# Kernel tuning notes

Hardware: AMD Instinct MI355X
Metric: run time of the kernel (lower is better)

The kernel has to match this reference:

```python
import jax, jax.numpy as jnp
import numpy as np

# SparseSphereConv (graph_level=6 -> V=40962, kernel_size=9, stride=1, select_index=None)
# Pipeline: neighbor gather -> data-dependent nonzero row selection ->
# per-vertex KxK interpolation matmul -> 1xK conv (linear over C_in,K) -> scatter back.
# With stride=1 / select_index=None the static selection is the identity, so the
# dynamic nonzero selection is equivalent to computing all rows and zeroing the
# rows whose gathered features are entirely zero (selected rows are scattered back,
# unselected rows stay 0 in sparse_reset's zero-initialized output).

BS, C_IN, C_OUT, V, K = 4, 32, 32, 40962, 9

def setup_inputs() -> dict:
    key = jax.random.key(0)
    k1, k2, k3, k4, k5 = jax.random.split(key, 5)
    x = jax.random.normal(k1, (BS, C_IN, V), dtype=jnp.float32)
    index = jax.random.randint(k2, (V, K), 0, V, dtype=jnp.int32)          # neighbor ids per vertex
    itp_mat = jax.random.uniform(k3, (V, K, K), dtype=jnp.float32)         # per-vertex interpolation
    conv_w = jax.random.normal(k4, (C_OUT, C_IN, K), dtype=jnp.float32) * 0.05  # Conv2d(C_in,C_out,(1,K)) weight
    conv_b = jax.random.normal(k5, (C_OUT,), dtype=jnp.float32) * 0.05
    return {"x": x, "index": index, "itp_mat": itp_mat, "conv_w": conv_w, "conv_b": conv_b}

def reference(x, index, itp_mat, conv_w, conv_b):
    # x: [bs, C, V] -> permute(2,0,1) -> gather neighbors -> [V, K, bs, C]
    g = jnp.transpose(x, (2, 0, 1))[index]
    g = jnp.transpose(g, (3, 2, 0, 1))                      # [C, bs, V, K]  (== reshape of [C, bs*V, K])
    # sparse_prepare: keep rows whose min or max over (C, K) is nonzero (detached in torch)
    gd = jax.lax.stop_gradient(g)
    rmin = gd.min(axis=(0, 3))                              # [bs, V]
    rmax = gd.max(axis=(0, 3))                              # [bs, V]
    mask = (rmin != 0) | (rmax != 0)                        # [bs, V]
    # Interploate: [C, S, 1, K] @ [S, K, K] per row -> batched small matmul
    interp = jnp.einsum('cbvk,vkj->cbvj', g, itp_mat)       # [C, bs, V, K]
    # Conv2d with kernel (1, K): contraction over (C_in, K) + bias
    out = jnp.einsum('cbvk,ock->bov', interp, conv_w) + conv_b[None, :, None]  # [bs, C_out, V]
    # sparse_reset: rows not selected stay zero
    return out * mask[:, None, :].astype(out.dtype)
```

## Files before the change

### kernel.cpp

```cpp
#include <hip/hip_runtime.h>

#define NV 40962
#define NK 9
#define CIN 32
#define COUT 32
#define NBS 4
#define VT 256
#define TP 260
#define NT 2561
#define PGRID 512
#define NV81 (NV * 81)
#define NV9  (NV * 9)

typedef __attribute__((ext_vector_type(8))) short bf16x8;
typedef __attribute__((ext_vector_type(4))) float f32x4;

__device__ __forceinline__ unsigned bf16pair(float a, float b) {
    unsigned ua = __float_as_uint(a), ub = __float_as_uint(b);
    ua = (ua + 0x7FFFu + ((ua >> 16) & 1u)) >> 16;
    ub = (ub + 0x7FFFu + ((ub >> 16) & 1u)) & 0xFFFF0000u;
    return (ua & 0xFFFFu) | ub;
}

__device__ __forceinline__ void bar_lgkm() {
    asm volatile("s_waitcnt lgkmcnt(0)\n\ts_barrier" ::: "memory");
}

__global__ void __launch_bounds__(256) transpose_x_bf16(
    const float* __restrict__ x, unsigned* __restrict__ xtw)
{
    __shared__ unsigned T[16 * TP];
    const int b  = blockIdx.x & 3;
    const int v0 = (blockIdx.x >> 2) * VT;
    const int t  = threadIdx.x;
    const int w  = t >> 6;
    const int L  = t & 63;
    const bool full = (v0 + VT <= NV);

    #pragma unroll
    for (int i = 0; i < 4; ++i) {
        const int q = w + 4 * i;
        const float* rowA = x + (size_t)(b * 32 + 2 * q) * NV;
        const float* rowB = rowA + NV;
        #pragma unroll
        for (int h = 0; h < 2; ++h) {
            const int vl = 128 * h + 2 * L;
            float2 a, c;
            if (full) {
                a = *(const float2*)(rowA + v0 + vl);
                c = *(const float2*)(rowB + v0 + vl);
            } else {
                const int v = v0 + vl;
                a.x = (v     < NV) ? rowA[v]     : 0.0f;
                a.y = (v + 1 < NV) ? rowA[v + 1] : 0.0f;
                c.x = (v     < NV) ? rowB[v]     : 0.0f;
                c.y = (v + 1 < NV) ? rowB[v + 1] : 0.0f;
            }
            uint2 d;
            d.x = bf16pair(a.x, c.x);
            d.y = bf16pair(a.y, c.y);
            *(uint2*)&T[q * TP + vl] = d;
        }
    }
    __syncthreads();

    #pragma unroll
    for (int i = 0; i < 4; ++i) {
        const int vl = i * 64 + w * 16 + (L >> 2);
        const int u4 = L & 3;
        const int v  = v0 + vl;
        if (v < NV) {
            uint4 d;
            d.x = T[(4 * u4 + 0) * TP + vl];
            d.y = T[(4 * u4 + 1) * TP + vl];
            d.z = T[(4 * u4 + 2) * TP + vl];
            d.w = T[(4 * u4 + 3) * TP + vl];
            *(uint4*)&xtw[(size_t)v * 64 + b * 16 + 4 * u4] = d;
        }
    }
}

__device__ __forceinline__ void load_itp(float itpv[3],
                                         const float* __restrict__ itp,
                                         int tile, int t)
{
    const size_t base = (size_t)tile * 1296;
    #pragma unroll
    for (int i = 0; i < 3; ++i) {
        const int o = i * 512 + t;
        itpv[i] = (o < 1296 && base + o < (size_t)NV81) ? itp[base + o] : 0.0f;
    }
}

__device__ __forceinline__ void stage_itp(float* __restrict__ buf,
                                          const float itpv[3], int t)
{
    #pragma unroll
    for (int i = 0; i < 3; ++i) {
        const int o = i * 512 + t;
        if (o < 1296) {
            const int vl = o / 81;
            const int r  = o - vl * 81;
            const int kk = r / 9;
            const int jj = r - kk * 9;
            buf[vl * 108 + kk * 12 + jj] = itpv[i];
        }
    }
}

__device__ __forceinline__ int load_idx(const int* __restrict__ index,
                                        int tile, int t)
{
    int r = 0;
    if (t < 144) {
        const size_t base = (size_t)tile * 144 + t;
        r = (base < (size_t)NV9) ? index[base] : 0;
    }
    return r;
}

__global__ void __launch_bounds__(512) sparse_conv_mfma(
    const unsigned short* __restrict__ xt, const int* __restrict__ index,
    const float* __restrict__ itp, const float* __restrict__ w,
    const float* __restrict__ bias, float* __restrict__ out)
{
    __shared__ unsigned short Alds[36 * 64 * 8];
    __shared__ unsigned short Wlds[36 * 32 * 8];
    __shared__ float itp_s[16 * 108];
    __shared__ int   idx_s[2][144];
    __shared__ unsigned nzv[8][64];

    const int t    = threadIdx.x;
    const int col  = t & 63;
    const int q    = t >> 6;
    const int b    = col >> 4;
    const int vloc = col & 15;
    const unsigned short* gb = xt + b * 32 + q * 4;

    int tile = blockIdx.x;

    #pragma unroll
    for (int r = 0; r < 3; ++r) {
        const int j = t + r * 512;
        if (j < 1152) {
            const int o = j & 31;
            const int c = j >> 5;
            const float4 f0 = *(const float4*)(w + o * 288 + c * 8);
            const float4 f1 = *(const float4*)(w + o * 288 + c * 8 + 4);
            uint4 d;
            d.x = bf16pair(f0.x, f0.y); d.y = bf16pair(f0.z, f0.w);
            d.z = bf16pair(f1.x, f1.y); d.w = bf16pair(f1.z, f1.w);
            *(uint4*)&Wlds[(c * 32 + o) * 8] = d;
        }
    }
    {
        const int i0 = load_idx(index, tile, t);
        const int i1 = load_idx(index, min(tile + PGRID, NT - 1), t);
        if (t < 144) { idx_s[0][t] = i0; idx_s[1][t] = i1; }
    }
    float itpv[3];
    load_itp(itpv, itp, tile, t);
    stage_itp(itp_s, itpv, t);
    bar_lgkm();

    uint2 gath[NK];
    #pragma unroll
    for (int k = 0; k < NK; ++k) {
        const int nbr = idx_s[0][vloc * 9 + k];
        gath[k] = *(const uint2*)(gb + (size_t)nbr * 128);
    }
    load_itp(itpv, itp, min(tile + PGRID, NT - 1), t);
    int idxn = load_idx(index, min(tile + 2 * PGRID, NT - 1), t);
    int cur = 0;

    for (; tile < NT; tile += PGRID) {
        unsigned nzbits = 0;
        float acc[4][NK];
        #pragma unroll
        for (int cc = 0; cc < 4; ++cc)
            #pragma unroll
            for (int j = 0; j < NK; ++j) acc[cc][j] = 0.0f;
        #pragma unroll
        for (int k = 0; k < NK; ++k) {
            const unsigned lo = gath[k].x, hi = gath[k].y;
            nzbits |= (lo | hi) & 0x7FFF7FFFu;
            const float g0 = __uint_as_float(lo << 16);
            const float g1 = __uint_as_float(lo & 0xFFFF0000u);
            const float g2 = __uint_as_float(hi << 16);
            const float g3 = __uint_as_float(hi & 0xFFFF0000u);
            const float4 ra = *(const float4*)&itp_s[vloc * 108 + k * 12];
            const float4 rb = *(const float4*)&itp_s[vloc * 108 + k * 12 + 4];
            const float  r8 = itp_s[vloc * 108 + k * 12 + 8];
            const float row[NK] = {ra.x, ra.y, ra.z, ra.w,
                                   rb.x, rb.y, rb.z, rb.w, r8};
            #pragma unroll
            for (int j = 0; j < NK; ++j) {
                acc[0][j] += g0 * row[j];
                acc[1][j] += g1 * row[j];
                acc[2][j] += g2 * row[j];
                acc[3][j] += g3 * row[j];
            }
        }
        #pragma unroll
        for (int i2 = 0; i2 < 9; ++i2) {
            const int k0 = 4 * i2;
            const int chunk = (9 * q + i2) >> 1;
            const int off = 4 * ((q + i2) & 1);
            uint2 d;
            d.x = bf16pair(acc[k0 / 9][k0 % 9],
                           acc[(k0 + 1) / 9][(k0 + 1) % 9]);
            d.y = bf16pair(acc[(k0 + 2) / 9][(k0 + 2) % 9],
                           acc[(k0 + 3) / 9][(k0 + 3) % 9]);
            *(uint2*)&Alds[(chunk * 64 + col) * 8 + off] = d;
        }
        nzv[q][col] = nzbits;

        #pragma unroll
        for (int k = 0; k < NK; ++k) {
            const int nbr = idx_s[cur ^ 1][vloc * 9 + k];
            gath[k] = *(const uint2*)(gb + (size_t)nbr * 128);
        }

        bar_lgkm();

        {
            const int dn = vloc;
            const int dq = col >> 4;
            const int bb = q >> 1;
            const int oh = q & 1;
            const int colw = bb * 16 + dn;

            f32x4 a0 = {0.f, 0.f, 0.f, 0.f};
            #pragma unroll
            for (int ks = 0; ks < 9; ++ks) {
                const int ch = ks * 4 + dq;
                const bf16x8 wa = *(const bf16x8*)&Wlds[(ch * 32 + oh * 16 + dn) * 8];
                const bf16x8 bf = *(const bf16x8*)&Alds[(ch * 64 + colw) * 8];
                a0 = __builtin_amdgcn_mfma_f32_16x16x32_bf16(wa, bf, a0, 0, 0, 0);
            }

            const unsigned nz = nzv[0][colw] | nzv[1][colw] |
                                nzv[2][colw] | nzv[3][colw] |
                                nzv[4][colw] | nzv[5][colw] |
                                nzv[6][colw] | nzv[7][colw];
            const float m = nz ? 1.0f : 0.0f;
            const int vv = tile * 16 + dn;
            if (vv < NV) {
                float* outb = out + (size_t)bb * (COUT * NV) + vv;
                #pragma unroll
                for (int r = 0; r < 4; ++r) {
                    const int o = oh * 16 + dq * 4 + r;
                    outb[(size_t)o * NV] = (a0[r] + bias[o]) * m;
                }
            }
        }
        stage_itp(itp_s, itpv, t);
        if (t < 144) idx_s[cur][t] = idxn;
        load_itp(itpv, itp, min(tile + 2 * PGRID, NT - 1), t);
        idxn = load_idx(index, min(tile + 3 * PGRID, NT - 1), t);

        bar_lgkm();
        cur ^= 1;
    }
}

extern "C" void kernel_launch(void* const* d_in, const int* in_sizes, int n_in,
                              void* d_out, int out_size, void* d_ws, size_t ws_size,
                              hipStream_t stream)
{
    const float* x     = (const float*)d_in[0];
    const int*   index = (const int*)  d_in[1];
    const float* itp   = (const float*)d_in[2];
    const float* w     = (const float*)d_in[3];
    const float* bias  = (const float*)d_in[4];
    float*       out   = (float*)d_out;

    unsigned short* xt = (unsigned short*)d_ws;

    const int vtiles = (NV + VT - 1) / VT;
    hipLaunchKernelGGL(transpose_x_bf16, dim3(vtiles * NBS), dim3(256), 0,
                       stream, x, (unsigned*)xt);
    hipLaunchKernelGGL(sparse_conv_mfma, dim3(PGRID), dim3(512), 0,
                       stream, xt, index, itp, w, bias, out);
}
```

Measured before the change: 139.7 us.

## Stage neighbor gathers via direct global-to-LDS DMA and keep weights in registers

Replaces the per-thread register gathers of neighbor rows with global_load_lds DMA into a double-buffered padded LDS tile, prefetching the next tile's rows while the current one is computed. Conv weight fragments move from LDS into per-thread registers, index storage shrinks to 16-bit, and the nonzero mask is reduced with a wave ballot instead of a per-lane LDS array. The persistent grid drops from 512 to 256 blocks to fit the larger LDS footprint. The trade-off is lower occupancy and a full barrier per iteration, plus higher register use from the weight fragments.

```diff
diff --git a/kernel.cpp b/kernel.cpp
--- a/kernel.cpp
+++ b/kernel.cpp
@@ -8,7 +8,8 @@
 #define VT 256
 #define TP 260
 #define NT 2561
-#define PGRID 512
+#define PGRID 256
+#define GROW 66
 #define NV81 (NV * 81)
 #define NV9  (NV * 9)
 
@@ -24,6 +25,12 @@
 
 __device__ __forceinline__ void bar_lgkm() {
     asm volatile("s_waitcnt lgkmcnt(0)\n\ts_barrier" ::: "memory");
+}
+
+__device__ __forceinline__ void dma_row4(const unsigned* g, unsigned* l) {
+    __builtin_amdgcn_global_load_lds(
+        (const __attribute__((address_space(1))) unsigned*)g,
+        (__attribute__((address_space(3))) unsigned*)l, 4, 0, 0);
 }
 
 __global__ void __launch_bounds__(256) transpose_x_bf16(
@@ -124,56 +131,65 @@
     const float* __restrict__ itp, const float* __restrict__ w,
     const float* __restrict__ bias, float* __restrict__ out)
 {
+    __shared__ unsigned Glds[2][144 * GROW];
     __shared__ unsigned short Alds[36 * 64 * 8];
-    __shared__ unsigned short Wlds[36 * 32 * 8];
     __shared__ float itp_s[16 * 108];
-    __shared__ int   idx_s[2][144];
-    __shared__ unsigned nzv[8][64];
+    __shared__ unsigned short idx_s[2][144];
+    __shared__ unsigned long long nzb[8];
 
     const int t    = threadIdx.x;
     const int col  = t & 63;
     const int q    = t >> 6;
     const int b    = col >> 4;
     const int vloc = col & 15;
-    const unsigned short* gb = xt + b * 32 + q * 4;
+    const unsigned* xtw = (const unsigned*)xt;
+
+    bf16x8 wfr[9];
+    {
+        const int o = (q & 1) * 16 + vloc;
+        const float* wo = w + o * 288 + b * 8;
+        #pragma unroll
+        for (int ks = 0; ks < 9; ++ks) {
+            const float4 f0 = *(const float4*)(wo + ks * 32);
+            const float4 f1 = *(const float4*)(wo + ks * 32 + 4);
+            union { uint4 u; bf16x8 v; } cv;
+            cv.u.x = bf16pair(f0.x, f0.y); cv.u.y = bf16pair(f0.z, f0.w);
+            cv.u.z = bf16pair(f1.x, f1.y); cv.u.w = bf16pair(f1.z, f1.w);
+            wfr[ks] = cv.v;
+        }
+    }
 
     int tile = blockIdx.x;
-
-    #pragma unroll
-    for (int r = 0; r < 3; ++r) {
-        const int j = t + r * 512;
-        if (j < 1152) {
-            const int o = j & 31;
-            const int c = j >> 5;
-            const float4 f0 = *(const float4*)(w + o * 288 + c * 8);
-            const float4 f1 = *(const float4*)(w + o * 288 + c * 8 + 4);
-            uint4 d;
-            d.x = bf16pair(f0.x, f0.y); d.y = bf16pair(f0.z, f0.w);
-            d.z = bf16pair(f1.x, f1.y); d.w = bf16pair(f1.z, f1.w);
-            *(uint4*)&Wlds[(c * 32 + o) * 8] = d;
-        }
-    }
     {
         const int i0 = load_idx(index, tile, t);
         const int i1 = load_idx(index, min(tile + PGRID, NT - 1), t);
-        if (t < 144) { idx_s[0][t] = i0; idx_s[1][t] = i1; }
+        if (t < 144) { idx_s[0][t] = (unsigned short)i0;
+                       idx_s[1][t] = (unsigned short)i1; }
     }
     float itpv[3];
     load_itp(itpv, itp, tile, t);
     stage_itp(itp_s, itpv, t);
-    bar_lgkm();
-
-    uint2 gath[NK];
-    #pragma unroll
-    for (int k = 0; k < NK; ++k) {
-        const int nbr = idx_s[0][vloc * 9 + k];
-        gath[k] = *(const uint2*)(gb + (size_t)nbr * 128);
+    __syncthreads();
+
+    #pragma unroll
+    for (int r = 0; r < 18; ++r) {
+        const int row = q * 18 + r;
+        const int nbr = idx_s[0][row];
+        dma_row4(xtw + (size_t)nbr * 64 + col, &Glds[0][row * GROW]);
     }
     load_itp(itpv, itp, min(tile + PGRID, NT - 1), t);
     int idxn = load_idx(index, min(tile + 2 * PGRID, NT - 1), t);
-    int cur = 0;
-
+    __syncthreads();
+
+    int g = 0, cur = 0;
     for (; tile < NT; tile += PGRID) {
+        #pragma unroll
+        for (int r = 0; r < 18; ++r) {
+            const int row = q * 18 + r;
+            const int nbr = idx_s[cur ^ 1][row];
+            dma_row4(xtw + (size_t)nbr * 64 + col, &Glds[g ^ 1][row * GROW]);
+        }
+
         unsigned nzbits = 0;
         float acc[4][NK];
         #pragma unroll
@@ -182,7 +198,8 @@
             for (int j = 0; j < NK; ++j) acc[cc][j] = 0.0f;
         #pragma unroll
         for (int k = 0; k < NK; ++k) {
-            const unsigned lo = gath[k].x, hi = gath[k].y;
+            const unsigned* p = &Glds[g][(vloc * 9 + k) * GROW + b * 16 + q * 2];
+            const unsigned lo = p[0], hi = p[1];
             nzbits |= (lo | hi) & 0x7FFF7FFFu;
             const float g0 = __uint_as_float(lo << 16);
             const float g1 = __uint_as_float(lo & 0xFFFF0000u);
@@ -213,38 +230,30 @@
                            acc[(k0 + 3) / 9][(k0 + 3) % 9]);
             *(uint2*)&Alds[(chunk * 64 + col) * 8 + off] = d;
         }
-        nzv[q][col] = nzbits;
-
-        #pragma unroll
-        for (int k = 0; k < NK; ++k) {
-            const int nbr = idx_s[cur ^ 1][vloc * 9 + k];
-            gath[k] = *(const uint2*)(gb + (size_t)nbr * 128);
-        }
+        const unsigned long long bal = __ballot(nzbits != 0);
+        if (col == 0) nzb[q] = bal;
 
         bar_lgkm();
 
         {
-            const int dn = vloc;
-            const int dq = col >> 4;
+            const int dq = b;
             const int bb = q >> 1;
             const int oh = q & 1;
-            const int colw = bb * 16 + dn;
+            const int colw = bb * 16 + vloc;
 
             f32x4 a0 = {0.f, 0.f, 0.f, 0.f};
             #pragma unroll
             for (int ks = 0; ks < 9; ++ks) {
                 const int ch = ks * 4 + dq;
-                const bf16x8 wa = *(const bf16x8*)&Wlds[(ch * 32 + oh * 16 + dn) * 8];
                 const bf16x8 bf = *(const bf16x8*)&Alds[(ch * 64 + colw) * 8];
-                a0 = __builtin_amdgcn_mfma_f32_16x16x32_bf16(wa, bf, a0, 0, 0, 0);
-            }
-
-            const unsigned nz = nzv[0][colw] | nzv[1][colw] |
-                                nzv[2][colw] | nzv[3][colw] |
-                                nzv[4][colw] | nzv[5][colw] |
-                                nzv[6][colw] | nzv[7][colw];
-            const float m = nz ? 1.0f : 0.0f;
-            const int vv = tile * 16 + dn;
+                a0 = __builtin_amdgcn_mfma_f32_16x16x32_bf16(wfr[ks], bf, a0,
+                                                             0, 0, 0);
+            }
+
+            const unsigned long long nz = nzb[0] | nzb[1] | nzb[2] | nzb[3] |
+                                          nzb[4] | nzb[5] | nzb[6] | nzb[7];
+            const float m = ((nz >> colw) & 1ull) ? 1.0f : 0.0f;
+            const int vv = tile * 16 + vloc;
             if (vv < NV) {
                 float* outb = out + (size_t)bb * (COUT * NV) + vv;
                 #pragma unroll
@@ -255,12 +264,12 @@
             }
         }
         stage_itp(itp_s, itpv, t);
-        if (t < 144) idx_s[cur][t] = idxn;
+        if (t < 144) idx_s[cur][t] = (unsigned short)idxn;
         load_itp(itpv, itp, min(tile + 2 * PGRID, NT - 1), t);
         idxn = load_idx(index, min(tile + 3 * PGRID, NT - 1), t);
 
-        bar_lgkm();
-        cur ^= 1;
+        __syncthreads();
+        g ^= 1; cur ^= 1;
     }
 }
 
```

After: 148.2 us. 6.1% more time.

## Interleave neighbor gathers with interpolation FMAs and compact LDS A-tile and nonzero mask

Applied to the files above, without the earlier changes.

Splits the per-tile consume loop so the next tile's neighbor gathers are issued after the first four and then the remaining five neighbors are consumed, overlapping global loads with the FMA work instead of issuing all loads after the pack stage. It also repacks the A tile in LDS into 8-byte half-chunks that are reassembled into 8-wide bf16 operands before the MFMA. The per-column nonzero words are replaced with a wavefront ballot stored as one 64-bit mask per wave. Hand-written bf16 rounding is swapped for the HIP bf16x2 conversion intrinsic. The trade-off is more LDS read instructions per MFMA and higher register pressure while gathers are in flight.

```diff
diff --git a/kernel.cpp b/kernel.cpp
--- a/kernel.cpp
+++ b/kernel.cpp
@@ -1,4 +1,5 @@
 #include <hip/hip_runtime.h>
+#include <hip/hip_bf16.h>
 
 #define NV 40962
 #define NK 9
@@ -15,11 +16,10 @@
 typedef __attribute__((ext_vector_type(8))) short bf16x8;
 typedef __attribute__((ext_vector_type(4))) float f32x4;
 
-__device__ __forceinline__ unsigned bf16pair(float a, float b) {
-    unsigned ua = __float_as_uint(a), ub = __float_as_uint(b);
-    ua = (ua + 0x7FFFu + ((ua >> 16) & 1u)) >> 16;
-    ub = (ub + 0x7FFFu + ((ub >> 16) & 1u)) & 0xFFFF0000u;
-    return (ua & 0xFFFFu) | ub;
+__device__ __forceinline__ unsigned pkbf(float a, float b) {
+    union { __hip_bfloat162 h2; unsigned u; } cv;
+    cv.h2 = __float22bfloat162_rn(make_float2(a, b));
+    return cv.u;
 }
 
 __device__ __forceinline__ void bar_lgkm() {
@@ -57,8 +57,8 @@
                 c.y = (v + 1 < NV) ? rowB[v + 1] : 0.0f;
             }
             uint2 d;
-            d.x = bf16pair(a.x, c.x);
-            d.y = bf16pair(a.y, c.y);
+            d.x = pkbf(a.x, c.x);
+            d.y = pkbf(a.y, c.y);
             *(uint2*)&T[q * TP + vl] = d;
         }
     }
@@ -119,16 +119,39 @@
     return r;
 }
 
+__device__ __forceinline__ void consume_k(const uint2 gk,
+                                          const float* __restrict__ irow,
+                                          float acc[4][NK], unsigned& nzbits)
+{
+    const unsigned lo = gk.x, hi = gk.y;
+    nzbits |= (lo | hi) & 0x7FFF7FFFu;
+    const float g0 = __uint_as_float(lo << 16);
+    const float g1 = __uint_as_float(lo & 0xFFFF0000u);
+    const float g2 = __uint_as_float(hi << 16);
+    const float g3 = __uint_as_float(hi & 0xFFFF0000u);
+    const float4 ra = *(const float4*)irow;
+    const float4 rb = *(const float4*)(irow + 4);
+    const float  rc = irow[8];
+    const float row[NK] = {ra.x, ra.y, ra.z, ra.w, rb.x, rb.y, rb.z, rb.w, rc};
+    #pragma unroll
+    for (int j = 0; j < NK; ++j) {
+        acc[0][j] += g0 * row[j];
+        acc[1][j] += g1 * row[j];
+        acc[2][j] += g2 * row[j];
+        acc[3][j] += g3 * row[j];
+    }
+}
+
 __global__ void __launch_bounds__(512) sparse_conv_mfma(
     const unsigned short* __restrict__ xt, const int* __restrict__ index,
     const float* __restrict__ itp, const float* __restrict__ w,
     const float* __restrict__ bias, float* __restrict__ out)
 {
-    __shared__ unsigned short Alds[36 * 64 * 8];
+    __shared__ unsigned Alds8[72 * 64 * 2];
     __shared__ unsigned short Wlds[36 * 32 * 8];
     __shared__ float itp_s[16 * 108];
     __shared__ int   idx_s[2][144];
-    __shared__ unsigned nzv[8][64];
+    __shared__ unsigned long long nzb[8];
 
     const int t    = threadIdx.x;
     const int col  = t & 63;
@@ -148,8 +171,8 @@
             const float4 f0 = *(const float4*)(w + o * 288 + c * 8);
             const float4 f1 = *(const float4*)(w + o * 288 + c * 8 + 4);
             uint4 d;
-            d.x = bf16pair(f0.x, f0.y); d.y = bf16pair(f0.z, f0.w);
-            d.z = bf16pair(f1.x, f1.y); d.w = bf16pair(f1.z, f1.w);
+            d.x = pkbf(f0.x, f0.y); d.y = pkbf(f0.z, f0.w);
+            d.z = pkbf(f1.x, f1.y); d.w = pkbf(f1.z, f1.w);
             *(uint4*)&Wlds[(c * 32 + o) * 8] = d;
         }
     }
@@ -161,7 +184,7 @@
     float itpv[3];
     load_itp(itpv, itp, tile, t);
     stage_itp(itp_s, itpv, t);
-    bar_lgkm();
+    __syncthreads();
 
     uint2 gath[NK];
     #pragma unroll
@@ -180,71 +203,62 @@
         for (int cc = 0; cc < 4; ++cc)
             #pragma unroll
             for (int j = 0; j < NK; ++j) acc[cc][j] = 0.0f;
-        #pragma unroll
-        for (int k = 0; k < NK; ++k) {
-            const unsigned lo = gath[k].x, hi = gath[k].y;
-            nzbits |= (lo | hi) & 0x7FFF7FFFu;
-            const float g0 = __uint_as_float(lo << 16);
-            const float g1 = __uint_as_float(lo & 0xFFFF0000u);
-            const float g2 = __uint_as_float(hi << 16);
-            const float g3 = __uint_as_float(hi & 0xFFFF0000u);
-            const float4 ra = *(const float4*)&itp_s[vloc * 108 + k * 12];
-            const float4 rb = *(const float4*)&itp_s[vloc * 108 + k * 12 + 4];
-            const float  r8 = itp_s[vloc * 108 + k * 12 + 8];
-            const float row[NK] = {ra.x, ra.y, ra.z, ra.w,
-                                   rb.x, rb.y, rb.z, rb.w, r8};
-            #pragma unroll
-            for (int j = 0; j < NK; ++j) {
-                acc[0][j] += g0 * row[j];
-                acc[1][j] += g1 * row[j];
-                acc[2][j] += g2 * row[j];
-                acc[3][j] += g3 * row[j];
-            }
-        }
+        const float* ib = &itp_s[vloc * 108];
+
+        #pragma unroll
+        for (int k = 0; k < 4; ++k) consume_k(gath[k], ib + k * 12, acc, nzbits);
+        #pragma unroll
+        for (int k = 0; k < 4; ++k) {
+            const int nbr = idx_s[cur ^ 1][vloc * 9 + k];
+            gath[k] = *(const uint2*)(gb + (size_t)nbr * 128);
+        }
+        #pragma unroll
+        for (int k = 4; k < 9; ++k) consume_k(gath[k], ib + k * 12, acc, nzbits);
+        #pragma unroll
+        for (int k = 4; k < 9; ++k) {
+            const int nbr = idx_s[cur ^ 1][vloc * 9 + k];
+            gath[k] = *(const uint2*)(gb + (size_t)nbr * 128);
+        }
+
         #pragma unroll
         for (int i2 = 0; i2 < 9; ++i2) {
             const int k0 = 4 * i2;
-            const int chunk = (9 * q + i2) >> 1;
-            const int off = 4 * ((q + i2) & 1);
+            const int h  = 9 * q + i2;
             uint2 d;
-            d.x = bf16pair(acc[k0 / 9][k0 % 9],
-                           acc[(k0 + 1) / 9][(k0 + 1) % 9]);
-            d.y = bf16pair(acc[(k0 + 2) / 9][(k0 + 2) % 9],
-                           acc[(k0 + 3) / 9][(k0 + 3) % 9]);
-            *(uint2*)&Alds[(chunk * 64 + col) * 8 + off] = d;
-        }
-        nzv[q][col] = nzbits;
-
-        #pragma unroll
-        for (int k = 0; k < NK; ++k) {
-            const int nbr = idx_s[cur ^ 1][vloc * 9 + k];
-            gath[k] = *(const uint2*)(gb + (size_t)nbr * 128);
-        }
+            d.x = pkbf(acc[k0 / 9][k0 % 9],
+                       acc[(k0 + 1) / 9][(k0 + 1) % 9]);
+            d.y = pkbf(acc[(k0 + 2) / 9][(k0 + 2) % 9],
+                       acc[(k0 + 3) / 9][(k0 + 3) % 9]);
+            *(uint2*)&Alds8[(h * 64 + col) * 2] = d;
+        }
+        const unsigned long long bal = __ballot(nzbits != 0);
+        if (col == 0) nzb[q] = bal;
 
         bar_lgkm();
 
         {
-            const int dn = vloc;
-            const int dq = col >> 4;
+            const int dq = b;
             const int bb = q >> 1;
             const int oh = q & 1;
-            const int colw = bb * 16 + dn;
+            const int colw = bb * 16 + vloc;
 
             f32x4 a0 = {0.f, 0.f, 0.f, 0.f};
             #pragma unroll
             for (int ks = 0; ks < 9; ++ks) {
+                const int h0 = ks * 8 + dq * 2;
+                const uint2 l2 = *(const uint2*)&Alds8[(h0 * 64 + colw) * 2];
+                const uint2 h2 = *(const uint2*)&Alds8[((h0 + 1) * 64 + colw) * 2];
+                union { uint4 u; bf16x8 v; } f;
+                f.u.x = l2.x; f.u.y = l2.y; f.u.z = h2.x; f.u.w = h2.y;
                 const int ch = ks * 4 + dq;
-                const bf16x8 wa = *(const bf16x8*)&Wlds[(ch * 32 + oh * 16 + dn) * 8];
-                const bf16x8 bf = *(const bf16x8*)&Alds[(ch * 64 + colw) * 8];
-                a0 = __builtin_amdgcn_mfma_f32_16x16x32_bf16(wa, bf, a0, 0, 0, 0);
+                const bf16x8 wa = *(const bf16x8*)&Wlds[(ch * 32 + oh * 16 + vloc) * 8];
+                a0 = __builtin_amdgcn_mfma_f32_16x16x32_bf16(wa, f.v, a0, 0, 0, 0);
             }
 
-            const unsigned nz = nzv[0][colw] | nzv[1][colw] |
-                                nzv[2][colw] | nzv[3][colw] |
-                                nzv[4][colw] | nzv[5][colw] |
-                                nzv[6][colw] | nzv[7][colw];
-            const float m = nz ? 1.0f : 0.0f;
-            const int vv = tile * 16 + dn;
+            const unsigned long long nz = nzb[0] | nzb[1] | nzb[2] | nzb[3] |
+                                          nzb[4] | nzb[5] | nzb[6] | nzb[7];
+            const float m = ((nz >> colw) & 1ull) ? 1.0f : 0.0f;
+            const int vv = tile * 16 + vloc;
             if (vv < NV) {
                 float* outb = out + (size_t)bb * (COUT * NV) + vv;
                 #pragma unroll
```

Result: no change. 139.7 us (-0.0%).
